# Performance work log

Hardware: AMD Instinct MI355X
Metric: run time of the kernel (lower is better)

Reference implementation:

```python
import jax, jax.numpy as jnp
import numpy as np

PATCH = 16
EMBED = 384
BINS = 32
LN_EPS = 1e-5


def setup_inputs() -> dict:
    key = jax.random.key(0)
    k1, k2 = jax.random.split(key, 2)
    images = jax.random.uniform(k1, (64, 3, 224, 224), dtype=jnp.float32)  # pixels in [0,1]
    proj_w = jax.random.normal(k2, (EMBED, 3, PATCH, PATCH), dtype=jnp.float32) * 0.02  # OIHW
    proj_b = jnp.zeros((EMBED,), jnp.float32)
    ln_gamma = jnp.ones((EMBED,), jnp.float32)
    ln_beta = jnp.zeros((EMBED,), jnp.float32)
    return {"images": images, "proj_w": proj_w, "proj_b": proj_b,
            "ln_gamma": ln_gamma, "ln_beta": ln_beta}


def _patch_entropy(images, patch_size):
    # images: (B, C, H, W) in [0,1]
    B, C, H, W = images.shape
    gH, gW = H // patch_size, W // patch_size
    gray = images.mean(axis=1)  # (B, H, W)
    # non-overlapping patches -> (B, N, P*P)
    patches = gray.reshape(B, gH, patch_size, gW, patch_size)
    patches = patches.transpose(0, 1, 3, 2, 4).reshape(B, gH * gW, patch_size * patch_size)
    # quantize to 32 bins (floor, matching torch .long() on non-negative values)
    q = jnp.clip(patches * (BINS - 1), 0, BINS - 1).astype(jnp.int32)
    one_hot = jax.nn.one_hot(q, BINS, dtype=jnp.float32)      # (B, N, P*P, 32)
    hist = one_hot.sum(axis=2)                                 # (B, N, 32)
    prob = hist / jnp.maximum(hist.sum(axis=-1, keepdims=True), 1e-8)
    log_prob = jnp.log2(prob + 1e-10)
    entropy = -(prob * log_prob).sum(axis=-1)                  # (B, N)
    return entropy / np.float32(np.log2(BINS))


def reference(images, proj_w, proj_b, ln_gamma, ln_beta):
    p = PATCH
    B, C, H, W = images.shape
    gH, gW = H // p, W // p
    entropy = _patch_entropy(images, p)
    # patch-embed conv: kernel=stride=patch_size, VALID padding
    x = jax.lax.conv_general_dilated(
        images, proj_w, window_strides=(p, p), padding='VALID',
        dimension_numbers=('NCHW', 'OIHW', 'NCHW'))            # (B, D, gH, gW)
    x = x + proj_b[None, :, None, None]
    x = x.transpose(0, 2, 3, 1).reshape(B, gH * gW, -1)        # (B, N, D)
    mu = x.mean(axis=-1, keepdims=True)
    var = x.var(axis=-1, keepdims=True)                        # biased, like torch LayerNorm
    x = (x - mu) / jnp.sqrt(var + LN_EPS) * ln_gamma + ln_beta
    return x, entropy
```

## Files before the change

### kernel.cpp

```cpp
#include <hip/hip_runtime.h>

#define BATCH 64
#define GH 14
#define GW 14
#define NPATCH (GH*GW)
#define M_ROWS (BATCH*NPATCH)
#define KDIM 768
#define DDIM 384
#define HW (224*224)

typedef __attribute__((ext_vector_type(8))) short s16x8;
typedef __attribute__((ext_vector_type(4))) float f32x4;
typedef __attribute__((ext_vector_type(4))) unsigned short u16x4;

__device__ __forceinline__ unsigned short f2bf(float f) {
    unsigned int u = __float_as_uint(f);
    u += 0x7fff + ((u >> 16) & 1);
    return (unsigned short)(u >> 16);
}

__device__ __forceinline__ void load_lds16(const void* g, void* l) {
    __builtin_amdgcn_global_load_lds(
        (const __attribute__((address_space(1))) unsigned int*)g,
        (__attribute__((address_space(3))) unsigned int*)l, 16, 0, 0);
}

__global__ __launch_bounds__(256) void wcast_kernel(const float* __restrict__ w,
                                                    unsigned short* __restrict__ W) {
    int t = blockIdx.x * 256 + threadIdx.x;
    float4 v = ((const float4*)w)[t];
    u16x4 o = { f2bf(v.x), f2bf(v.y), f2bf(v.z), f2bf(v.w) };
    *(u16x4*)(W + t * 4) = o;
}

__global__ __launch_bounds__(256) void im2col_kernel(const float* __restrict__ img,
                                                     unsigned short* __restrict__ A) {
    int t = blockIdx.x * 256 + threadIdx.x;
    float4 v = ((const float4*)img)[t];
    int x4   = t % 56;
    int rest = t / 56;
    int y    = rest % 224;
    int bc   = rest / 224;
    int b = bc / 3, c = bc - 3 * b;
    int ph = y >> 4, r = y & 15;
    int pw = x4 >> 2, col = (x4 & 3) * 4;
    int row = b * NPATCH + ph * GW + pw;
    int k   = c * 256 + r * 16 + col;
    u16x4 o = { f2bf(v.x), f2bf(v.y), f2bf(v.z), f2bf(v.w) };
    *(u16x4*)(A + row * KDIM + k) = o;
}

__global__ __launch_bounds__(256) void entropy_kernel(const float* __restrict__ img,
                                                      float* __restrict__ ent) {
    __shared__ int hist[4][32];
    const int lane = threadIdx.x & 63;
    const int wave = threadIdx.x >> 6;
    const int p = blockIdx.x * 4 + wave;
    const int b = p / NPATCH;
    const int n = p - b * NPATCH;
    const int ph = n / GW, pw = n - ph * GW;

    if (lane < 32) hist[wave][lane] = 0;
    __syncthreads();

    const float* base = img + b * (3 * HW) + (ph * 16) * 224 + pw * 16;
#pragma unroll
    for (int j = 0; j < 4; ++j) {
        int idx = lane + 64 * j;
        int r = idx >> 4, cc = idx & 15;
        const float* px = base + r * 224 + cc;
        float g = (px[0] + px[HW] + px[2 * HW]) / 3.0f;
        int bin = (int)(g * 31.0f);
        bin = bin < 0 ? 0 : (bin > 31 ? 31 : bin);
        atomicAdd(&hist[wave][bin], 1);
    }
    __syncthreads();

    float t = 0.0f;
    if (lane < 32) {
        float pr = (float)hist[wave][lane] * (1.0f / 256.0f);
        t = -pr * log2f(pr + 1e-10f);
    }
#pragma unroll
    for (int off = 32; off; off >>= 1) t += __shfl_xor(t, off);
    if (lane == 0) ent[p] = t * (1.0f / 5.0f);
}

__global__ __launch_bounds__(256) void gemm_kernel(const unsigned short* __restrict__ A,
                                                   const unsigned short* __restrict__ Bt,
                                                   const float* __restrict__ bias,
                                                   float* __restrict__ C) {
    __shared__ __align__(16) unsigned short As[128 * 64];
    __shared__ __align__(16) unsigned short Bs[128 * 64];
    const int tid  = threadIdx.x;
    const int lane = tid & 63;
    const int wave = tid >> 6;
    const int wm = wave >> 1, wn = wave & 1;
    const int rowBase = blockIdx.y * 128;
    const int colBase = blockIdx.x * 128;

    f32x4 acc[4][4] = {};

    for (int kt = 0; kt < KDIM; kt += 64) {
#pragma unroll
        for (int i = 0; i < 4; ++i) {
            int f = i * 256 + tid;
            int r = f >> 3, ks = f & 7;
            load_lds16(A  + (rowBase + r) * KDIM + kt + ks * 8, (unsigned short*)As + f * 8);
            load_lds16(Bt + (colBase + r) * KDIM + kt + ks * 8, (unsigned short*)Bs + f * 8);
        }
        __syncthreads();
#pragma unroll
        for (int ks = 0; ks < 2; ++ks) {
            const int ko = ks * 32 + (lane >> 4) * 8;
            s16x8 a_frag[4], b_frag[4];
#pragma unroll
            for (int i = 0; i < 4; ++i) {
                int m = wm * 64 + i * 16 + (lane & 15);
                a_frag[i] = *(const s16x8*)(As + m * 64 + ko);
                int n = wn * 64 + i * 16 + (lane & 15);
                b_frag[i] = *(const s16x8*)(Bs + n * 64 + ko);
            }
#pragma unroll
            for (int i = 0; i < 4; ++i)
#pragma unroll
                for (int j = 0; j < 4; ++j)
                    acc[i][j] = __builtin_amdgcn_mfma_f32_16x16x32_bf16(
                        a_frag[i], b_frag[j], acc[i][j], 0, 0, 0);
        }
        __syncthreads();
    }

    const int quad = lane >> 4;
    const int cl = lane & 15;
#pragma unroll
    for (int j = 0; j < 4; ++j) {
        int col = colBase + wn * 64 + j * 16 + cl;
        float bv = bias[col];
#pragma unroll
        for (int i = 0; i < 4; ++i) {
            int row0 = rowBase + wm * 64 + i * 16 + quad * 4;
#pragma unroll
            for (int r = 0; r < 4; ++r)
                C[(size_t)(row0 + r) * DDIM + col] = acc[i][j][r] + bv;
        }
    }
}

__global__ __launch_bounds__(256) void ln_kernel(float* __restrict__ X,
                                                 const float* __restrict__ gamma,
                                                 const float* __restrict__ beta) {
    __shared__ float sg[DDIM], sb[DDIM];
    for (int i = threadIdx.x; i < DDIM; i += 256) { sg[i] = gamma[i]; sb[i] = beta[i]; }
    __syncthreads();
    const int lane = threadIdx.x & 63;
    const int wave = threadIdx.x >> 6;
    const int row = blockIdx.x * 4 + wave;
    float* x = X + (size_t)row * DDIM + lane * 6;

    float2 p0 = *(float2*)(x);
    float2 p1 = *(float2*)(x + 2);
    float2 p2 = *(float2*)(x + 4);
    float v[6] = { p0.x, p0.y, p1.x, p1.y, p2.x, p2.y };

    float s = v[0] + v[1] + v[2] + v[3] + v[4] + v[5];
#pragma unroll
    for (int off = 32; off; off >>= 1) s += __shfl_xor(s, off);
    float mean = s * (1.0f / (float)DDIM);

    float d = 0.0f;
#pragma unroll
    for (int j = 0; j < 6; ++j) { float t = v[j] - mean; d += t * t; }
#pragma unroll
    for (int off = 32; off; off >>= 1) d += __shfl_xor(d, off);
    float rstd = 1.0f / sqrtf(d * (1.0f / (float)DDIM) + 1e-5f);

    const float* g = sg + lane * 6;
    const float* b = sb + lane * 6;
#pragma unroll
    for (int j = 0; j < 6; ++j) x[j] = (v[j] - mean) * rstd * g[j] + b[j];
}

extern "C" void kernel_launch(void* const* d_in, const int* in_sizes, int n_in,
                              void* d_out, int out_size, void* d_ws, size_t ws_size,
                              hipStream_t stream) {
    const float* img = (const float*)d_in[0];
    const float* pw  = (const float*)d_in[1];
    const float* pb  = (const float*)d_in[2];
    const float* gam = (const float*)d_in[3];
    const float* bet = (const float*)d_in[4];
    float* out = (float*)d_out;

    unsigned short* Abf = (unsigned short*)d_ws;
    unsigned short* Wbf = (unsigned short*)((char*)d_ws + 19267584);
    float* ent = out + (size_t)M_ROWS * DDIM;

    hipLaunchKernelGGL(wcast_kernel,   dim3(288),    dim3(256), 0, stream, pw, Wbf);
    hipLaunchKernelGGL(im2col_kernel,  dim3(9408),   dim3(256), 0, stream, img, Abf);
    hipLaunchKernelGGL(entropy_kernel, dim3(3136),   dim3(256), 0, stream, img, ent);
    hipLaunchKernelGGL(gemm_kernel,    dim3(3, 98),  dim3(256), 0, stream, Abf, Wbf, pb, out);
    hipLaunchKernelGGL(ln_kernel,      dim3(3136),   dim3(256), 0, stream, out, gam, bet);
}
```

Baseline: 132.1 us.

## Fuse im2col with entropy and shrink GEMM tiles to single-wave 64x64 blocks

```diff
diff --git a/kernel.cpp b/kernel.cpp
--- a/kernel.cpp
+++ b/kernel.cpp
@@ -33,25 +33,9 @@
     *(u16x4*)(W + t * 4) = o;
 }
 
-__global__ __launch_bounds__(256) void im2col_kernel(const float* __restrict__ img,
-                                                     unsigned short* __restrict__ A) {
-    int t = blockIdx.x * 256 + threadIdx.x;
-    float4 v = ((const float4*)img)[t];
-    int x4   = t % 56;
-    int rest = t / 56;
-    int y    = rest % 224;
-    int bc   = rest / 224;
-    int b = bc / 3, c = bc - 3 * b;
-    int ph = y >> 4, r = y & 15;
-    int pw = x4 >> 2, col = (x4 & 3) * 4;
-    int row = b * NPATCH + ph * GW + pw;
-    int k   = c * 256 + r * 16 + col;
-    u16x4 o = { f2bf(v.x), f2bf(v.y), f2bf(v.z), f2bf(v.w) };
-    *(u16x4*)(A + row * KDIM + k) = o;
-}
-
-__global__ __launch_bounds__(256) void entropy_kernel(const float* __restrict__ img,
-                                                      float* __restrict__ ent) {
+__global__ __launch_bounds__(256) void patch_kernel(const float* __restrict__ img,
+                                                    unsigned short* __restrict__ A,
+                                                    float* __restrict__ ent) {
     __shared__ int hist[4][32];
     const int lane = threadIdx.x & 63;
     const int wave = threadIdx.x >> 6;
@@ -63,14 +47,29 @@
     if (lane < 32) hist[wave][lane] = 0;
     __syncthreads();
 
-    const float* base = img + b * (3 * HW) + (ph * 16) * 224 + pw * 16;
+    const int r = lane >> 2;
+    const int cc = (lane & 3) * 4;
+    const float* base = img + (size_t)b * (3 * HW) + (ph * 16 + r) * 224 + pw * 16 + cc;
+
+    float4 v0 = *(const float4*)(base);
+    float4 v1 = *(const float4*)(base + HW);
+    float4 v2 = *(const float4*)(base + 2 * HW);
+
+    unsigned short* arow = A + (size_t)p * KDIM;
+    u16x4 o0 = { f2bf(v0.x), f2bf(v0.y), f2bf(v0.z), f2bf(v0.w) };
+    u16x4 o1 = { f2bf(v1.x), f2bf(v1.y), f2bf(v1.z), f2bf(v1.w) };
+    u16x4 o2 = { f2bf(v2.x), f2bf(v2.y), f2bf(v2.z), f2bf(v2.w) };
+    *(u16x4*)(arow + 0 * 256 + lane * 4) = o0;
+    *(u16x4*)(arow + 1 * 256 + lane * 4) = o1;
+    *(u16x4*)(arow + 2 * 256 + lane * 4) = o2;
+
+    float g[4] = { (v0.x + v1.x + v2.x) / 3.0f,
+                   (v0.y + v1.y + v2.y) / 3.0f,
+                   (v0.z + v1.z + v2.z) / 3.0f,
+                   (v0.w + v1.w + v2.w) / 3.0f };
 #pragma unroll
     for (int j = 0; j < 4; ++j) {
-        int idx = lane + 64 * j;
-        int r = idx >> 4, cc = idx & 15;
-        const float* px = base + r * 224 + cc;
-        float g = (px[0] + px[HW] + px[2 * HW]) / 3.0f;
-        int bin = (int)(g * 31.0f);
+        int bin = (int)(g[j] * 31.0f);
         bin = bin < 0 ? 0 : (bin > 31 ? 31 : bin);
         atomicAdd(&hist[wave][bin], 1);
     }
@@ -86,28 +85,25 @@
     if (lane == 0) ent[p] = t * (1.0f / 5.0f);
 }
 
-__global__ __launch_bounds__(256) void gemm_kernel(const unsigned short* __restrict__ A,
-                                                   const unsigned short* __restrict__ Bt,
-                                                   const float* __restrict__ bias,
-                                                   float* __restrict__ C) {
-    __shared__ __align__(16) unsigned short As[128 * 64];
-    __shared__ __align__(16) unsigned short Bs[128 * 64];
-    const int tid  = threadIdx.x;
-    const int lane = tid & 63;
-    const int wave = tid >> 6;
-    const int wm = wave >> 1, wn = wave & 1;
-    const int rowBase = blockIdx.y * 128;
-    const int colBase = blockIdx.x * 128;
+__global__ __launch_bounds__(64) void gemm_kernel(const unsigned short* __restrict__ A,
+                                                  const unsigned short* __restrict__ Bt,
+                                                  const float* __restrict__ bias,
+                                                  float* __restrict__ C) {
+    __shared__ __align__(16) unsigned short As[64 * 64];
+    __shared__ __align__(16) unsigned short Bs[64 * 64];
+    const int lane = threadIdx.x;
+    const int rowBase = blockIdx.y * 64;
+    const int colBase = blockIdx.x * 64;
 
     f32x4 acc[4][4] = {};
 
     for (int kt = 0; kt < KDIM; kt += 64) {
 #pragma unroll
-        for (int i = 0; i < 4; ++i) {
-            int f = i * 256 + tid;
+        for (int i = 0; i < 8; ++i) {
+            int f = i * 64 + lane;
             int r = f >> 3, ks = f & 7;
-            load_lds16(A  + (rowBase + r) * KDIM + kt + ks * 8, (unsigned short*)As + f * 8);
-            load_lds16(Bt + (colBase + r) * KDIM + kt + ks * 8, (unsigned short*)Bs + f * 8);
+            load_lds16(A  + (size_t)(rowBase + r) * KDIM + kt + ks * 8, (unsigned short*)As + f * 8);
+            load_lds16(Bt + (size_t)(colBase + r) * KDIM + kt + ks * 8, (unsigned short*)Bs + f * 8);
         }
         __syncthreads();
 #pragma unroll
@@ -116,10 +112,8 @@
             s16x8 a_frag[4], b_frag[4];
 #pragma unroll
             for (int i = 0; i < 4; ++i) {
-                int m = wm * 64 + i * 16 + (lane & 15);
-                a_frag[i] = *(const s16x8*)(As + m * 64 + ko);
-                int n = wn * 64 + i * 16 + (lane & 15);
-                b_frag[i] = *(const s16x8*)(Bs + n * 64 + ko);
+                a_frag[i] = *(const s16x8*)(As + (i * 16 + (lane & 15)) * 64 + ko);
+                b_frag[i] = *(const s16x8*)(Bs + (i * 16 + (lane & 15)) * 64 + ko);
             }
 #pragma unroll
             for (int i = 0; i < 4; ++i)
@@ -135,11 +129,11 @@
     const int cl = lane & 15;
 #pragma unroll
     for (int j = 0; j < 4; ++j) {
-        int col = colBase + wn * 64 + j * 16 + cl;
+        int col = colBase + j * 16 + cl;
         float bv = bias[col];
 #pragma unroll
         for (int i = 0; i < 4; ++i) {
-            int row0 = rowBase + wm * 64 + i * 16 + quad * 4;
+            int row0 = rowBase + i * 16 + quad * 4;
 #pragma unroll
             for (int r = 0; r < 4; ++r)
                 C[(size_t)(row0 + r) * DDIM + col] = acc[i][j][r] + bv;
@@ -195,9 +189,8 @@
     unsigned short* Wbf = (unsigned short*)((char*)d_ws + 19267584);
     float* ent = out + (size_t)M_ROWS * DDIM;
 
-    hipLaunchKernelGGL(wcast_kernel,   dim3(288),    dim3(256), 0, stream, pw, Wbf);
-    hipLaunchKernelGGL(im2col_kernel,  dim3(9408),   dim3(256), 0, stream, img, Abf);
-    hipLaunchKernelGGL(entropy_kernel, dim3(3136),   dim3(256), 0, stream, img, ent);
-    hipLaunchKernelGGL(gemm_kernel,    dim3(3, 98),  dim3(256), 0, stream, Abf, Wbf, pb, out);
-    hipLaunchKernelGGL(ln_kernel,      dim3(3136),   dim3(256), 0, stream, out, gam, bet);
+    hipLaunchKernelGGL(wcast_kernel, dim3(288),      dim3(256), 0, stream, pw, Wbf);
+    hipLaunchKernelGGL(patch_kernel, dim3(3136),     dim3(256), 0, stream, img, Abf, ent);
+    hipLaunchKernelGGL(gemm_kernel,  dim3(6, 196),   dim3(64),  0, stream, Abf, Wbf, pb, out);
+    hipLaunchKernelGGL(ln_kernel,    dim3(3136),     dim3(256), 0, stream, out, gam, bet);
 }
```

New measurement: 123.4 us. -6.6%, faster.
